# Optimization experiments

Hardware: AMD Instinct MI355X
Metric: run time of the kernel (lower is better)

The kernel has to match this reference:

```python
import jax, jax.numpy as jnp
import numpy as np

GI_DIM = 1220
HID = 150
GIJ = 3 * GI_DIM + 60  # 3720


def setup_inputs() -> dict:
    key = jax.random.key(0)
    ks = jax.random.split(key, 16)
    N, P = 50000, 100000
    inp = {
        "g_i": jax.random.normal(ks[0], (N, GI_DIM), jnp.float32),
        "mention_scores": jax.random.normal(ks[1], (N,), jnp.float32),
        "dist_emb": jax.random.normal(ks[2], (9, 20), jnp.float32) * 0.1,
        "genre_emb": jax.random.normal(ks[3], (8, 20), jnp.float32) * 0.1,
        "speaker_emb": jax.random.normal(ks[4], (3, 20), jnp.float32) * 0.1,
        "W1": jax.random.normal(ks[5], (GIJ, HID), jnp.float32) / np.sqrt(GIJ),
        "b1": jnp.zeros((HID,), jnp.float32),
        "W2": jax.random.normal(ks[6], (HID, HID), jnp.float32) / np.sqrt(HID),
        "b2": jnp.zeros((HID,), jnp.float32),
        "W3": jax.random.normal(ks[7], (HID, 1), jnp.float32) / np.sqrt(HID),
        "b3": jnp.zeros((1,), jnp.float32),
        "mention_ids": jax.random.randint(ks[8], (P,), 0, N, jnp.int64 if jax.config.jax_enable_x64 else jnp.int32),
        "antecedent_ids": jax.random.randint(ks[9], (P,), 0, N, jnp.int32),
        "distance_ids": jax.random.randint(ks[10], (P,), 0, 9, jnp.int32),
        "genre_ids": jax.random.randint(ks[11], (P,), 0, 8, jnp.int32),
        "speaker_ids": jax.random.randint(ks[12], (P,), 0, 3, jnp.int32),
    }
    return inp


def reference(g_i, mention_scores, dist_emb, genre_emb, speaker_emb,
              W1, b1, W2, b2, W3, b3,
              mention_ids, antecedent_ids, distance_ids, genre_ids, speaker_ids):
    # phi: [P, 60] pair features (distance, genre, speaker embeddings)
    phi = jnp.concatenate([dist_emb[distance_ids],
                           genre_emb[genre_ids],
                           speaker_emb[speaker_ids]], axis=1)
    i_g = g_i[mention_ids]      # [P, GI_DIM]
    j_g = g_i[antecedent_ids]   # [P, GI_DIM]
    pairs = jnp.concatenate([i_g, j_g, i_g * j_g, phi], axis=1)  # [P, GIJ]
    h = jax.nn.relu(pairs @ W1 + b1)
    h = jax.nn.relu(h @ W2 + b2)
    pairwise = (h @ W3 + b3)[:, 0]  # [P]
    sij = mention_scores[mention_ids] + mention_scores[antecedent_ids] + pairwise
    return sij
```

## Files before the change

kernel.cpp:

```cpp
#include <hip/hip_runtime.h>

#define GI  1220
#define KP  1280
#define BK  128
#define NCH (KP / BK)
#define NP  192
#define ABW 320

typedef _Float16      f16;
typedef _Float16      f16x8 __attribute__((ext_vector_type(8)));
typedef float         f32x4 __attribute__((ext_vector_type(4)));
typedef unsigned int  u32x4 __attribute__((ext_vector_type(4)));
typedef unsigned int  u32x2 __attribute__((ext_vector_type(2)));

__device__ __forceinline__ unsigned short f2h(float f) {
  return __builtin_bit_cast(unsigned short, (f16)f);
}
__device__ __forceinline__ float h2f(unsigned short u) {
  return (float)__builtin_bit_cast(f16, u);
}
__device__ __forceinline__ unsigned int pkh(float a, float b) {
  return (unsigned int)f2h(a) | ((unsigned int)f2h(b) << 16);
}

__global__ void prep_kernel(const float* __restrict__ W1, const float* __restrict__ W2,
                            const float* __restrict__ b1,
                            const float* __restrict__ de, const float* __restrict__ ge,
                            const float* __restrict__ se,
                            unsigned short* __restrict__ W1ab_t,
                            unsigned short* __restrict__ W1c_t,
                            unsigned short* __restrict__ W2_t,
                            float* __restrict__ projs) {
  int idx = blockIdx.x * 256 + threadIdx.x;
  const int R1 = ABW * KP, R2 = NP * KP, R3 = NP * NP, R4 = 20 * NP;
  if (idx < R1) {
    int n = idx / KP, k = idx % KP;
    float v = 0.f;
    if (k < GI) {
      if (n < 150)                 v = W1[k * 150 + n];
      else if (n >= 160 && n < 310) v = W1[(GI + k) * 150 + (n - 160)];
    }
    W1ab_t[idx] = f2h(v);
    return;
  }
  idx -= R1;
  if (idx < R2) {
    int n = idx / KP, k = idx % KP;
    float v = (k < GI && n < 150) ? W1[(2 * GI + k) * 150 + n] : 0.f;
    W1c_t[idx] = f2h(v);
    return;
  }
  idx -= R2;
  if (idx < R3) {
    int n = idx / NP, k = idx % NP;
    float v = (n < 150 && k < 150) ? W2[k * 150 + n] : 0.f;
    W2_t[idx] = f2h(v);
    return;
  }
  idx -= R3;
  if (idx < R4) {
    int r = idx / NP, n = idx % NP;
    float v = 0.f;
    if (n < 150) {
      if (r < 9) {
        v = b1[n];
        for (int t = 0; t < 20; ++t) v += de[r * 20 + t] * W1[(3660 + t) * 150 + n];
      } else if (r < 17) {
        int q = r - 9;
        for (int t = 0; t < 20; ++t) v += ge[q * 20 + t] * W1[(3680 + t) * 150 + n];
      } else {
        int q = r - 17;
        for (int t = 0; t < 20; ++t) v += se[q * 20 + t] * W1[(3700 + t) * 150 + n];
      }
    }
    projs[idx] = v;
  }
}

__global__ __launch_bounds__(256, 3)
void ab_kernel(const float* __restrict__ g, const unsigned short* __restrict__ W1ab_t,
               unsigned short* __restrict__ AB, unsigned short* __restrict__ gb, int N) {
  __shared__ __attribute__((aligned(16))) unsigned short sX[64 * 136];
  const int t = threadIdx.x;
  const int m0 = blockIdx.x * 64;
  const int w = t >> 6, lane = t & 63, quad = lane >> 4, lm = lane & 15;

  f32x4 acc[4][5];
#pragma unroll
  for (int a = 0; a < 4; ++a)
#pragma unroll
    for (int b = 0; b < 5; ++b) { acc[a][b].x = 0.f; acc[a][b].y = 0.f; acc[a][b].z = 0.f; acc[a][b].w = 0.f; }

  const int r = t >> 2, s = t & 3;
  int row = m0 + r; if (row >= N) row = N - 1;
  const float* gr = g + (long)row * GI;
  unsigned short* gbr = gb + (long)row * KP;

  for (int c = 0; c < NCH; ++c) {
    __syncthreads();
#pragma unroll
    for (int i = 0; i < 8; ++i) {
      int k = c * BK + i * 16 + s * 4;
      u32x2 ph; ph.x = 0u; ph.y = 0u;
      if (k < GI) {
        f32x4 x = *(const f32x4*)(gr + k);
        ph.x = pkh(x.x, x.y);
        ph.y = pkh(x.z, x.w);
      }
      *(u32x2*)&sX[r * 136 + i * 16 + s * 4] = ph;
      *(u32x2*)(gbr + k) = ph;
    }
    __syncthreads();
#pragma unroll
    for (int kk = 0; kk < 4; ++kk) {
      f16x8 af[4];
#pragma unroll
      for (int mi = 0; mi < 4; ++mi)
        af[mi] = __builtin_bit_cast(f16x8, *(const u32x4*)&sX[(mi * 16 + lm) * 136 + kk * 32 + quad * 8]);
#pragma unroll
      for (int tl = 0; tl < 5; ++tl) {
        int n = (w * 5 + tl) * 16 + lm;
        f16x8 bfr = __builtin_bit_cast(f16x8, *(const u32x4*)(W1ab_t + n * KP + c * BK + kk * 32 + quad * 8));
#pragma unroll
        for (int mi = 0; mi < 4; ++mi)
          acc[mi][tl] = __builtin_amdgcn_mfma_f32_16x16x32_f16(af[mi], bfr, acc[mi][tl], 0, 0, 0);
      }
    }
  }
#pragma unroll
  for (int mi = 0; mi < 4; ++mi)
#pragma unroll
    for (int reg = 0; reg < 4; ++reg) {
      int m = m0 + mi * 16 + quad * 4 + reg;
      if (m < N) {
#pragma unroll
        for (int tl = 0; tl < 5; ++tl) {
          int n = (w * 5 + tl) * 16 + lm;
          AB[(long)m * ABW + n] = f2h(acc[mi][tl][reg]);
        }
      }
    }
}

__global__ __launch_bounds__(256, 3)
void pair_kernel(const unsigned short* __restrict__ gb, const float* __restrict__ msc,
                 const unsigned short* __restrict__ AB,
                 const unsigned short* __restrict__ W1c_t,
                 const unsigned short* __restrict__ W2_t,
                 const float* __restrict__ projs,
                 const float* __restrict__ b2, const float* __restrict__ W3,
                 const float* __restrict__ b3,
                 const int* __restrict__ mid, const int* __restrict__ aid,
                 const int* __restrict__ did, const int* __restrict__ gid,
                 const int* __restrict__ sid,
                 float* __restrict__ out, int N, int P) {
  __shared__ __attribute__((aligned(16))) unsigned short sXh1[64 * 200];
  __shared__ __attribute__((aligned(16))) unsigned short sBias[64 * NP];
  __shared__ int sM[64], sA[64], sD[64], sG[64], sS[64];
  __shared__ float sScore[64];

  const int t = threadIdx.x;
  const int p0 = blockIdx.x * 64;
  const int w = t >> 6, lane = t & 63, quad = lane >> 4, lm = lane & 15;

  if (t < 64) {
    int p = p0 + t;
    int m_ = 0, a_ = 0, d_ = 0, g_ = 0, s_ = 0;
    float sc = 0.f;
    if (p < P) {
      m_ = mid[p]; a_ = aid[p]; d_ = did[p]; g_ = gid[p]; s_ = sid[p];
      sc = msc[m_] + msc[a_];
    }
    sM[t] = m_; sA[t] = a_; sD[t] = d_; sG[t] = g_; sS[t] = s_;
    sScore[t] = sc;
  }
  __syncthreads();

  const int r = t >> 2, s = t & 3;
  const unsigned short* gbm = gb + (long)sM[r] * KP;
  const unsigned short* gba = gb + (long)sA[r] * KP;

  {
    const unsigned short* Ar = AB + (long)sM[r] * ABW;
    const unsigned short* Br = AB + (long)sA[r] * ABW + 160;
    const float* dp = projs + sD[r] * NP;
    const float* gp = projs + (9 + sG[r]) * NP;
    const float* sp = projs + (17 + sS[r]) * NP;
#pragma unroll
    for (int j = 0; j < 6; ++j) {
      int n = s * 48 + j * 8;
      f32x4 p0v = *(const f32x4*)(dp + n) + *(const f32x4*)(gp + n) + *(const f32x4*)(sp + n);
      f32x4 p1v = *(const f32x4*)(dp + n + 4) + *(const f32x4*)(gp + n + 4) + *(const f32x4*)(sp + n + 4);
      if (n < 160) {
        u32x4 a8 = *(const u32x4*)(Ar + n);
        u32x4 b8 = *(const u32x4*)(Br + n);
        p0v.x += h2f((unsigned short)(a8.x & 0xffff)) + h2f((unsigned short)(b8.x & 0xffff));
        p0v.y += h2f((unsigned short)(a8.x >> 16))    + h2f((unsigned short)(b8.x >> 16));
        p0v.z += h2f((unsigned short)(a8.y & 0xffff)) + h2f((unsigned short)(b8.y & 0xffff));
        p0v.w += h2f((unsigned short)(a8.y >> 16))    + h2f((unsigned short)(b8.y >> 16));
        p1v.x += h2f((unsigned short)(a8.z & 0xffff)) + h2f((unsigned short)(b8.z & 0xffff));
        p1v.y += h2f((unsigned short)(a8.z >> 16))    + h2f((unsigned short)(b8.z >> 16));
        p1v.z += h2f((unsigned short)(a8.w & 0xffff)) + h2f((unsigned short)(b8.w & 0xffff));
        p1v.w += h2f((unsigned short)(a8.w >> 16))    + h2f((unsigned short)(b8.w >> 16));
      }
      u32x4 o;
      o.x = pkh(p0v.x, p0v.y); o.y = pkh(p0v.z, p0v.w);
      o.z = pkh(p1v.x, p1v.y); o.w = pkh(p1v.z, p1v.w);
      *(u32x4*)&sBias[r * NP + n] = o;
    }
  }

  f32x4 acc[4][3];
#pragma unroll
  for (int a = 0; a < 4; ++a)
#pragma unroll
    for (int b = 0; b < 3; ++b) { acc[a][b].x = 0.f; acc[a][b].y = 0.f; acc[a][b].z = 0.f; acc[a][b].w = 0.f; }

  for (int c = 0; c < NCH; ++c) {
    __syncthreads();
#pragma unroll
    for (int i = 0; i < 4; ++i) {
      int k = c * BK + i * 32 + s * 8;
      f16x8 xm = __builtin_bit_cast(f16x8, *(const u32x4*)(gbm + k));
      f16x8 xa = __builtin_bit_cast(f16x8, *(const u32x4*)(gba + k));
      f16x8 pm = xm * xa;
      *(u32x4*)&sXh1[r * 136 + i * 32 + s * 8] = __builtin_bit_cast(u32x4, pm);
    }
    __syncthreads();
#pragma unroll
    for (int kk = 0; kk < 4; ++kk) {
      f16x8 af[4];
#pragma unroll
      for (int mi = 0; mi < 4; ++mi)
        af[mi] = __builtin_bit_cast(f16x8, *(const u32x4*)&sXh1[(mi * 16 + lm) * 136 + kk * 32 + quad * 8]);
#pragma unroll
      for (int tl = 0; tl < 3; ++tl) {
        int n = (w * 3 + tl) * 16 + lm;
        f16x8 bfr = __builtin_bit_cast(f16x8, *(const u32x4*)(W1c_t + n * KP + c * BK + kk * 32 + quad * 8));
#pragma unroll
        for (int mi = 0; mi < 4; ++mi)
          acc[mi][tl] = __builtin_amdgcn_mfma_f32_16x16x32_f16(af[mi], bfr, acc[mi][tl], 0, 0, 0);
      }
    }
  }

  __syncthreads();
#pragma unroll
  for (int mi = 0; mi < 4; ++mi)
#pragma unroll
    for (int tl = 0; tl < 3; ++tl) {
      int n = (w * 3 + tl) * 16 + lm;
#pragma unroll
      for (int reg = 0; reg < 4; ++reg) {
        int m = mi * 16 + quad * 4 + reg;
        float v = acc[mi][tl][reg] + h2f(sBias[m * NP + n]);
        v = fmaxf(v, 0.f);
        sXh1[m * 200 + n] = f2h(v);
      }
    }
  __syncthreads();

  f32x4 acc2[4][3];
#pragma unroll
  for (int a = 0; a < 4; ++a)
#pragma unroll
    for (int b = 0; b < 3; ++b) { acc2[a][b].x = 0.f; acc2[a][b].y = 0.f; acc2[a][b].z = 0.f; acc2[a][b].w = 0.f; }
#pragma unroll
  for (int kk = 0; kk < 6; ++kk) {
    f16x8 af[4];
#pragma unroll
    for (int mi = 0; mi < 4; ++mi)
      af[mi] = __builtin_bit_cast(f16x8, *(const u32x4*)&sXh1[(mi * 16 + lm) * 200 + kk * 32 + quad * 8]);
#pragma unroll
    for (int tl = 0; tl < 3; ++tl) {
      int n = (w * 3 + tl) * 16 + lm;
      f16x8 bfr = __builtin_bit_cast(f16x8, *(const u32x4*)(W2_t + n * NP + kk * 32 + quad * 8));
#pragma unroll
      for (int mi = 0; mi < 4; ++mi)
        acc2[mi][tl] = __builtin_amdgcn_mfma_f32_16x16x32_f16(af[mi], bfr, acc2[mi][tl], 0, 0, 0);
    }
  }

#pragma unroll
  for (int mi = 0; mi < 4; ++mi)
#pragma unroll
    for (int tl = 0; tl < 3; ++tl) {
      int n = (w * 3 + tl) * 16 + lm;
      float bb = (n < 150) ? b2[n] : 0.f;
#pragma unroll
      for (int reg = 0; reg < 4; ++reg) {
        int m = mi * 16 + quad * 4 + reg;
        float v = acc2[mi][tl][reg] + bb;
        v = fmaxf(v, 0.f);
        sBias[m * NP + n] = f2h(v);
      }
    }
  __syncthreads();

  {
    float sum = 0.f;
#pragma unroll
    for (int j = 0; j < 48; ++j) {
      int n = s * 48 + j;
      if (n < 150) sum += h2f(sBias[r * NP + n]) * W3[n];
    }
    sum += __shfl_xor(sum, 1);
    sum += __shfl_xor(sum, 2);
    if (s == 0) {
      int p = p0 + r;
      if (p < P) out[p] = sScore[r] + sum + b3[0];
    }
  }
}

extern "C" void kernel_launch(void* const* d_in, const int* in_sizes, int n_in,
                              void* d_out, int out_size, void* d_ws, size_t ws_size,
                              hipStream_t stream) {
  (void)n_in; (void)out_size; (void)ws_size;
  const float* g   = (const float*)d_in[0];
  const float* msc = (const float*)d_in[1];
  const float* de  = (const float*)d_in[2];
  const float* ge  = (const float*)d_in[3];
  const float* se  = (const float*)d_in[4];
  const float* W1  = (const float*)d_in[5];
  const float* b1  = (const float*)d_in[6];
  const float* W2  = (const float*)d_in[7];
  const float* b2  = (const float*)d_in[8];
  const float* W3  = (const float*)d_in[9];
  const float* b3  = (const float*)d_in[10];
  const int* mid = (const int*)d_in[11];
  const int* aid = (const int*)d_in[12];
  const int* did = (const int*)d_in[13];
  const int* gid = (const int*)d_in[14];
  const int* sid = (const int*)d_in[15];
  const int N = in_sizes[0] / GI;
  const int P = in_sizes[11];
  float* out = (float*)d_out;

  char* ws = (char*)d_ws;
  size_t off = 0;
  auto alloc = [&](size_t bytes) { char* p = ws + off; off = (off + bytes + 255) & ~(size_t)255; return p; };
  unsigned short* gb     = (unsigned short*)alloc((size_t)N * KP * 2);
  unsigned short* AB     = (unsigned short*)alloc((size_t)N * ABW * 2);
  unsigned short* W1ab_t = (unsigned short*)alloc((size_t)ABW * KP * 2);
  unsigned short* W1c_t  = (unsigned short*)alloc((size_t)NP * KP * 2);
  unsigned short* W2_t   = (unsigned short*)alloc((size_t)NP * NP * 2);
  float* projs           = (float*)alloc((size_t)20 * NP * 4);

  const int prep_total = ABW * KP + NP * KP + NP * NP + 20 * NP;
  prep_kernel<<<(prep_total + 255) / 256, 256, 0, stream>>>(W1, W2, b1, de, ge, se,
                                                            W1ab_t, W1c_t, W2_t, projs);
  ab_kernel<<<(N + 63) / 64, 256, 0, stream>>>(g, W1ab_t, AB, gb, N);
  pair_kernel<<<(P + 63) / 64, 256, 0, stream>>>(gb, msc, AB, W1c_t, W2_t, projs,
                                                 b2, W3, b3, mid, aid, did, gid, sid,
                                                 out, N, P);
}
```

Measured before the change: 781.5 us.

## Split fp16 conversion kernel, double-buffer ab_kernel, register-direct pair GEMM with prefetch

Moves the fp32-to-fp16 conversion of g into its own g2h kernel, so ab_kernel now reads fp16 rows and double-buffers them in shared memory with a single barrier per chunk. In pair_kernel, the elementwise product of gathered rows no longer goes through shared memory. Each wave loads its own 16 pair rows straight into registers as MFMA A fragments, with the next chunk prefetched, and computes all 12 N-tiles. This removes two barriers per K-chunk and the LDS round-trip. The cost is an extra kernel launch, an extra pass over g, more registers for 12 accumulators, and less reuse of W1c loads across rows.

Measured after the change: 1.032 ms. +32.1%, slower.

```diff
diff --git a/kernel.cpp b/kernel.cpp
--- a/kernel.cpp
+++ b/kernel.cpp
@@ -21,6 +21,29 @@
 }
 __device__ __forceinline__ unsigned int pkh(float a, float b) {
   return (unsigned int)f2h(a) | ((unsigned int)f2h(b) << 16);
+}
+
+__global__ void g2h_kernel(const float* __restrict__ g, unsigned short* __restrict__ gb,
+                           int N) {
+  int idx = blockIdx.x * 256 + threadIdx.x;
+  if (idx >= N * (KP / 8)) return;
+  int row = idx / (KP / 8);
+  int k = (idx % (KP / 8)) * 8;
+  const float* gr = g + (long)row * GI + k;
+  u32x4 o;
+  if (k + 8 <= GI) {
+    f32x4 a = *(const f32x4*)gr;
+    f32x4 b = *(const f32x4*)(gr + 4);
+    o.x = pkh(a.x, a.y); o.y = pkh(a.z, a.w);
+    o.z = pkh(b.x, b.y); o.w = pkh(b.z, b.w);
+  } else if (k < GI) {
+    f32x4 a = *(const f32x4*)gr;
+    o.x = pkh(a.x, a.y); o.y = pkh(a.z, a.w);
+    o.z = 0u; o.w = 0u;
+  } else {
+    o.x = 0u; o.y = 0u; o.z = 0u; o.w = 0u;
+  }
+  *(u32x4*)(gb + (long)row * KP + k) = o;
 }
 
 __global__ void prep_kernel(const float* __restrict__ W1, const float* __restrict__ W2,
@@ -78,9 +101,10 @@
 }
 
 __global__ __launch_bounds__(256, 3)
-void ab_kernel(const float* __restrict__ g, const unsigned short* __restrict__ W1ab_t,
-               unsigned short* __restrict__ AB, unsigned short* __restrict__ gb, int N) {
-  __shared__ __attribute__((aligned(16))) unsigned short sX[64 * 136];
+void ab_kernel(const unsigned short* __restrict__ gb,
+               const unsigned short* __restrict__ W1ab_t,
+               unsigned short* __restrict__ AB, int N) {
+  __shared__ __attribute__((aligned(16))) unsigned short sX[2][64 * 136];
   const int t = threadIdx.x;
   const int m0 = blockIdx.x * 64;
   const int w = t >> 6, lane = t & 63, quad = lane >> 4, lm = lane & 15;
@@ -93,39 +117,37 @@
 
   const int r = t >> 2, s = t & 3;
   int row = m0 + r; if (row >= N) row = N - 1;
-  const float* gr = g + (long)row * GI;
-  unsigned short* gbr = gb + (long)row * KP;
+  const unsigned short* gr = gb + (long)row * KP;
+
+#pragma unroll
+  for (int q = 0; q < 4; ++q)
+    *(u32x4*)&sX[0][r * 136 + s * 32 + q * 8] = *(const u32x4*)(gr + s * 32 + q * 8);
+  __syncthreads();
 
   for (int c = 0; c < NCH; ++c) {
-    __syncthreads();
-#pragma unroll
-    for (int i = 0; i < 8; ++i) {
-      int k = c * BK + i * 16 + s * 4;
-      u32x2 ph; ph.x = 0u; ph.y = 0u;
-      if (k < GI) {
-        f32x4 x = *(const f32x4*)(gr + k);
-        ph.x = pkh(x.x, x.y);
-        ph.y = pkh(x.z, x.w);
-      }
-      *(u32x2*)&sX[r * 136 + i * 16 + s * 4] = ph;
-      *(u32x2*)(gbr + k) = ph;
-    }
-    __syncthreads();
+    const int cur = c & 1;
+    if (c + 1 < NCH) {
+#pragma unroll
+      for (int q = 0; q < 4; ++q)
+        *(u32x4*)&sX[cur ^ 1][r * 136 + s * 32 + q * 8] =
+            *(const u32x4*)(gr + (c + 1) * BK + s * 32 + q * 8);
+    }
 #pragma unroll
     for (int kk = 0; kk < 4; ++kk) {
       f16x8 af[4];
 #pragma unroll
       for (int mi = 0; mi < 4; ++mi)
-        af[mi] = __builtin_bit_cast(f16x8, *(const u32x4*)&sX[(mi * 16 + lm) * 136 + kk * 32 + quad * 8]);
+        af[mi] = *(const f16x8*)&sX[cur][(mi * 16 + lm) * 136 + kk * 32 + quad * 8];
 #pragma unroll
       for (int tl = 0; tl < 5; ++tl) {
         int n = (w * 5 + tl) * 16 + lm;
-        f16x8 bfr = __builtin_bit_cast(f16x8, *(const u32x4*)(W1ab_t + n * KP + c * BK + kk * 32 + quad * 8));
+        f16x8 bfr = *(const f16x8*)(W1ab_t + n * KP + c * BK + kk * 32 + quad * 8);
 #pragma unroll
         for (int mi = 0; mi < 4; ++mi)
           acc[mi][tl] = __builtin_amdgcn_mfma_f32_16x16x32_f16(af[mi], bfr, acc[mi][tl], 0, 0, 0);
       }
     }
+    __syncthreads();
   }
 #pragma unroll
   for (int mi = 0; mi < 4; ++mi)
@@ -140,6 +162,27 @@
         }
       }
     }
+}
+
+__device__ __forceinline__ void pref(const unsigned short* pm, const unsigned short* pa,
+                                     int ko, f16x8 (&xm)[4], f16x8 (&xa)[4]) {
+#pragma unroll
+  for (int kk = 0; kk < 4; ++kk) {
+    xm[kk] = *(const f16x8*)(pm + ko + kk * 32);
+    xa[kk] = *(const f16x8*)(pa + ko + kk * 32);
+  }
+}
+__device__ __forceinline__ void comp(const unsigned short* __restrict__ W1c_t, int lm, int ko,
+                                     f16x8 (&xm)[4], f16x8 (&xa)[4], f32x4 (&acc)[12]) {
+#pragma unroll
+  for (int kk = 0; kk < 4; ++kk) {
+    f16x8 af = xm[kk] * xa[kk];
+#pragma unroll
+    for (int tl = 0; tl < 12; ++tl) {
+      f16x8 bf = *(const f16x8*)(W1c_t + (tl * 16 + lm) * KP + ko + kk * 32);
+      acc[tl] = __builtin_amdgcn_mfma_f32_16x16x32_f16(af, bf, acc[tl], 0, 0, 0);
+    }
+  }
 }
 
 __global__ __launch_bounds__(256, 3)
@@ -154,7 +197,7 @@
                  const int* __restrict__ did, const int* __restrict__ gid,
                  const int* __restrict__ sid,
                  float* __restrict__ out, int N, int P) {
-  __shared__ __attribute__((aligned(16))) unsigned short sXh1[64 * 200];
+  __shared__ __attribute__((aligned(16))) unsigned short sH1[64 * 200];
   __shared__ __attribute__((aligned(16))) unsigned short sBias[64 * NP];
   __shared__ int sM[64], sA[64], sD[64], sG[64], sS[64];
   __shared__ float sScore[64];
@@ -177,8 +220,6 @@
   __syncthreads();
 
   const int r = t >> 2, s = t & 3;
-  const unsigned short* gbm = gb + (long)sM[r] * KP;
-  const unsigned short* gba = gb + (long)sA[r] * KP;
 
   {
     const unsigned short* Ar = AB + (long)sM[r] * ABW;
@@ -210,71 +251,54 @@
     }
   }
 
-  f32x4 acc[4][3];
+  const int prow = w * 16 + lm;
+  const unsigned short* pm = gb + (long)sM[prow] * KP;
+  const unsigned short* pa = gb + (long)sA[prow] * KP;
+
+  f32x4 acc[12];
+#pragma unroll
+  for (int tl = 0; tl < 12; ++tl) { acc[tl].x = 0.f; acc[tl].y = 0.f; acc[tl].z = 0.f; acc[tl].w = 0.f; }
+
+  const int qo = quad * 8;
+  f16x8 xm0[4], xa0[4], xm1[4], xa1[4];
+  pref(pm, pa, qo, xm0, xa0);
+#pragma unroll
+  for (int c = 0; c < NCH; c += 2) {
+    if (c + 1 < NCH) pref(pm, pa, (c + 1) * BK + qo, xm1, xa1);
+    comp(W1c_t, lm, c * BK + qo, xm0, xa0, acc);
+    if (c + 2 < NCH) pref(pm, pa, (c + 2) * BK + qo, xm0, xa0);
+    if (c + 1 < NCH) comp(W1c_t, lm, (c + 1) * BK + qo, xm1, xa1, acc);
+  }
+
+  __syncthreads();
+#pragma unroll
+  for (int tl = 0; tl < 12; ++tl) {
+    int n = tl * 16 + lm;
+#pragma unroll
+    for (int reg = 0; reg < 4; ++reg) {
+      int m = w * 16 + quad * 4 + reg;
+      float v = acc[tl][reg] + h2f(sBias[m * NP + n]);
+      v = fmaxf(v, 0.f);
+      sH1[m * 200 + n] = f2h(v);
+    }
+  }
+  __syncthreads();
+
+  f32x4 acc2[4][3];
 #pragma unroll
   for (int a = 0; a < 4; ++a)
 #pragma unroll
-    for (int b = 0; b < 3; ++b) { acc[a][b].x = 0.f; acc[a][b].y = 0.f; acc[a][b].z = 0.f; acc[a][b].w = 0.f; }
-
-  for (int c = 0; c < NCH; ++c) {
-    __syncthreads();
-#pragma unroll
-    for (int i = 0; i < 4; ++i) {
-      int k = c * BK + i * 32 + s * 8;
-      f16x8 xm = __builtin_bit_cast(f16x8, *(const u32x4*)(gbm + k));
-      f16x8 xa = __builtin_bit_cast(f16x8, *(const u32x4*)(gba + k));
-      f16x8 pm = xm * xa;
-      *(u32x4*)&sXh1[r * 136 + i * 32 + s * 8] = __builtin_bit_cast(u32x4, pm);
-    }
-    __syncthreads();
-#pragma unroll
-    for (int kk = 0; kk < 4; ++kk) {
-      f16x8 af[4];
-#pragma unroll
-      for (int mi = 0; mi < 4; ++mi)
-        af[mi] = __builtin_bit_cast(f16x8, *(const u32x4*)&sXh1[(mi * 16 + lm) * 136 + kk * 32 + quad * 8]);
-#pragma unroll
-      for (int tl = 0; tl < 3; ++tl) {
-        int n = (w * 3 + tl) * 16 + lm;
-        f16x8 bfr = __builtin_bit_cast(f16x8, *(const u32x4*)(W1c_t + n * KP + c * BK + kk * 32 + quad * 8));
-#pragma unroll
-        for (int mi = 0; mi < 4; ++mi)
-          acc[mi][tl] = __builtin_amdgcn_mfma_f32_16x16x32_f16(af[mi], bfr, acc[mi][tl], 0, 0, 0);
-      }
-    }
-  }
-
-  __syncthreads();
-#pragma unroll
-  for (int mi = 0; mi < 4; ++mi)
+    for (int b = 0; b < 3; ++b) { acc2[a][b].x = 0.f; acc2[a][b].y = 0.f; acc2[a][b].z = 0.f; acc2[a][b].w = 0.f; }
+#pragma unroll
+  for (int kk = 0; kk < 6; ++kk) {
+    f16x8 af[4];
+#pragma unroll
+    for (int mi = 0; mi < 4; ++mi)
+      af[mi] = *(const f16x8*)&sH1[(mi * 16 + lm) * 200 + kk * 32 + qo];
 #pragma unroll
     for (int tl = 0; tl < 3; ++tl) {
       int n = (w * 3 + tl) * 16 + lm;
-#pragma unroll
-      for (int reg = 0; reg < 4; ++reg) {
-        int m = mi * 16 + quad * 4 + reg;
-        float v = acc[mi][tl][reg] + h2f(sBias[m * NP + n]);
-        v = fmaxf(v, 0.f);
-        sXh1[m * 200 + n] = f2h(v);
-      }
-    }
-  __syncthreads();
-
-  f32x4 acc2[4][3];
-#pragma unroll
-  for (int a = 0; a < 4; ++a)
-#pragma unroll
-    for (int b = 0; b < 3; ++b) { acc2[a][b].x = 0.f; acc2[a][b].y = 0.f; acc2[a][b].z = 0.f; acc2[a][b].w = 0.f; }
-#pragma unroll
-  for (int kk = 0; kk < 6; ++kk) {
-    f16x8 af[4];
-#pragma unroll
-    for (int mi = 0; mi < 4; ++mi)
-      af[mi] = __builtin_bit_cast(f16x8, *(const u32x4*)&sXh1[(mi * 16 + lm) * 200 + kk * 32 + quad * 8]);
-#pragma unroll
-    for (int tl = 0; tl < 3; ++tl) {
-      int n = (w * 3 + tl) * 16 + lm;
-      f16x8 bfr = __builtin_bit_cast(f16x8, *(const u32x4*)(W2_t + n * NP + kk * 32 + quad * 8));
+      f16x8 bfr = *(const f16x8*)(W2_t + n * NP + kk * 32 + qo);
 #pragma unroll
       for (int mi = 0; mi < 4; ++mi)
         acc2[mi][tl] = __builtin_amdgcn_mfma_f32_16x16x32_f16(af[mi], bfr, acc2[mi][tl], 0, 0, 0);
@@ -350,7 +374,8 @@
   const int prep_total = ABW * KP + NP * KP + NP * NP + 20 * NP;
   prep_kernel<<<(prep_total + 255) / 256, 256, 0, stream>>>(W1, W2, b1, de, ge, se,
                                                             W1ab_t, W1c_t, W2_t, projs);
-  ab_kernel<<<(N + 63) / 64, 256, 0, stream>>>(g, W1ab_t, AB, gb, N);
+  g2h_kernel<<<(N * (KP / 8) + 255) / 256, 256, 0, stream>>>(g, gb, N);
+  ab_kernel<<<(N + 63) / 64, 256, 0, stream>>>(gb, W1ab_t, AB, N);
   pair_kernel<<<(P + 63) / 64, 256, 0, stream>>>(gb, msc, AB, W1c_t, W2_t, projs,
                                                  b2, W3, b3, mid, aid, did, gid, sid,
                                                  out, N, P);
```

## Split fp16 conversion into own kernel and double-buffer ab/pair GEMM loads

Applied to the files above, without the earlier changes.

Moves the fp32-to-fp16 conversion of g_i out of ab_kernel into a separate g2h_kernel. ab_kernel then reads the fp16 copy with a register-prefetched, double-buffered LDS pipeline. pair_kernel's gathered-row loop now prefetches the next chunk's mention and antecedent rows into registers while the current chunk's MFMAs run, aiming to hide global gather latency. This costs an extra kernel launch, a second read of the fp16 g buffer, and more registers, which may lower occupancy under launch_bounds(256,3).

New measurement: 730.8 us. 1.07x faster.

```diff
diff --git a/kernel.cpp b/kernel.cpp
--- a/kernel.cpp
+++ b/kernel.cpp
@@ -21,6 +21,29 @@
 }
 __device__ __forceinline__ unsigned int pkh(float a, float b) {
   return (unsigned int)f2h(a) | ((unsigned int)f2h(b) << 16);
+}
+
+__global__ void g2h_kernel(const float* __restrict__ g, unsigned short* __restrict__ gb,
+                           int N) {
+  int idx = blockIdx.x * 256 + threadIdx.x;
+  if (idx >= N * (KP / 8)) return;
+  int row = idx / (KP / 8);
+  int k = (idx % (KP / 8)) * 8;
+  const float* gr = g + (long)row * GI + k;
+  u32x4 o;
+  if (k + 8 <= GI) {
+    f32x4 a = *(const f32x4*)gr;
+    f32x4 b = *(const f32x4*)(gr + 4);
+    o.x = pkh(a.x, a.y); o.y = pkh(a.z, a.w);
+    o.z = pkh(b.x, b.y); o.w = pkh(b.z, b.w);
+  } else if (k < GI) {
+    f32x4 a = *(const f32x4*)gr;
+    o.x = pkh(a.x, a.y); o.y = pkh(a.z, a.w);
+    o.z = 0u; o.w = 0u;
+  } else {
+    o.x = 0u; o.y = 0u; o.z = 0u; o.w = 0u;
+  }
+  *(u32x4*)(gb + (long)row * KP + k) = o;
 }
 
 __global__ void prep_kernel(const float* __restrict__ W1, const float* __restrict__ W2,
@@ -78,9 +101,10 @@
 }
 
 __global__ __launch_bounds__(256, 3)
-void ab_kernel(const float* __restrict__ g, const unsigned short* __restrict__ W1ab_t,
-               unsigned short* __restrict__ AB, unsigned short* __restrict__ gb, int N) {
-  __shared__ __attribute__((aligned(16))) unsigned short sX[64 * 136];
+void ab_kernel(const unsigned short* __restrict__ gb,
+               const unsigned short* __restrict__ W1ab_t,
+               unsigned short* __restrict__ AB, int N) {
+  __shared__ __attribute__((aligned(16))) unsigned short sX[2][64 * 136];
   const int t = threadIdx.x;
   const int m0 = blockIdx.x * 64;
   const int w = t >> 6, lane = t & 63, quad = lane >> 4, lm = lane & 15;
@@ -93,40 +117,46 @@
 
   const int r = t >> 2, s = t & 3;
   int row = m0 + r; if (row >= N) row = N - 1;
-  const float* gr = g + (long)row * GI;
-  unsigned short* gbr = gb + (long)row * KP;
+  const unsigned short* gr = gb + (long)row * KP;
+
+  u32x4 xr[4];
+  auto loadx = [&](int c) {
+#pragma unroll
+    for (int q = 0; q < 4; ++q)
+      xr[q] = *(const u32x4*)(gr + c * BK + s * 32 + q * 8);
+  };
+  auto storex = [&](int buf) {
+#pragma unroll
+    for (int q = 0; q < 4; ++q)
+      *(u32x4*)&sX[buf][r * 136 + s * 32 + q * 8] = xr[q];
+  };
+
+  loadx(0);
+  storex(0);
+  __syncthreads();
 
   for (int c = 0; c < NCH; ++c) {
-    __syncthreads();
-#pragma unroll
-    for (int i = 0; i < 8; ++i) {
-      int k = c * BK + i * 16 + s * 4;
-      u32x2 ph; ph.x = 0u; ph.y = 0u;
-      if (k < GI) {
-        f32x4 x = *(const f32x4*)(gr + k);
-        ph.x = pkh(x.x, x.y);
-        ph.y = pkh(x.z, x.w);
-      }
-      *(u32x2*)&sX[r * 136 + i * 16 + s * 4] = ph;
-      *(u32x2*)(gbr + k) = ph;
-    }
-    __syncthreads();
+    const int cur = c & 1;
+    if (c + 1 < NCH) loadx(c + 1);
 #pragma unroll
     for (int kk = 0; kk < 4; ++kk) {
       f16x8 af[4];
 #pragma unroll
       for (int mi = 0; mi < 4; ++mi)
-        af[mi] = __builtin_bit_cast(f16x8, *(const u32x4*)&sX[(mi * 16 + lm) * 136 + kk * 32 + quad * 8]);
+        af[mi] = *(const f16x8*)&sX[cur][(mi * 16 + lm) * 136 + kk * 32 + quad * 8];
 #pragma unroll
       for (int tl = 0; tl < 5; ++tl) {
         int n = (w * 5 + tl) * 16 + lm;
-        f16x8 bfr = __builtin_bit_cast(f16x8, *(const u32x4*)(W1ab_t + n * KP + c * BK + kk * 32 + quad * 8));
+        f16x8 bfr = *(const f16x8*)(W1ab_t + n * KP + c * BK + kk * 32 + quad * 8);
 #pragma unroll
         for (int mi = 0; mi < 4; ++mi)
           acc[mi][tl] = __builtin_amdgcn_mfma_f32_16x16x32_f16(af[mi], bfr, acc[mi][tl], 0, 0, 0);
       }
     }
-  }
+    if (c + 1 < NCH) storex(cur ^ 1);
+    __syncthreads();
+  }
+
 #pragma unroll
   for (int mi = 0; mi < 4; ++mi)
 #pragma unroll
@@ -216,32 +246,52 @@
 #pragma unroll
     for (int b = 0; b < 3; ++b) { acc[a][b].x = 0.f; acc[a][b].y = 0.f; acc[a][b].z = 0.f; acc[a][b].w = 0.f; }
 
-  for (int c = 0; c < NCH; ++c) {
-    __syncthreads();
+  u32x4 xm0[4], xa0[4], xm1[4], xa1[4];
+  auto loadc = [&](int c, u32x4 (&xm)[4], u32x4 (&xa)[4]) {
 #pragma unroll
     for (int i = 0; i < 4; ++i) {
-      int k = c * BK + i * 32 + s * 8;
-      f16x8 xm = __builtin_bit_cast(f16x8, *(const u32x4*)(gbm + k));
-      f16x8 xa = __builtin_bit_cast(f16x8, *(const u32x4*)(gba + k));
-      f16x8 pm = xm * xa;
+      xm[i] = *(const u32x4*)(gbm + c * BK + i * 32 + s * 8);
+      xa[i] = *(const u32x4*)(gba + c * BK + i * 32 + s * 8);
+    }
+  };
+  auto storec = [&](u32x4 (&xm)[4], u32x4 (&xa)[4]) {
+#pragma unroll
+    for (int i = 0; i < 4; ++i) {
+      f16x8 pm = __builtin_bit_cast(f16x8, xm[i]) * __builtin_bit_cast(f16x8, xa[i]);
       *(u32x4*)&sXh1[r * 136 + i * 32 + s * 8] = __builtin_bit_cast(u32x4, pm);
     }
-    __syncthreads();
+  };
+  auto mfmac = [&](int c) {
 #pragma unroll
     for (int kk = 0; kk < 4; ++kk) {
       f16x8 af[4];
 #pragma unroll
       for (int mi = 0; mi < 4; ++mi)
-        af[mi] = __builtin_bit_cast(f16x8, *(const u32x4*)&sXh1[(mi * 16 + lm) * 136 + kk * 32 + quad * 8]);
+        af[mi] = *(const f16x8*)&sXh1[(mi * 16 + lm) * 136 + kk * 32 + quad * 8];
 #pragma unroll
       for (int tl = 0; tl < 3; ++tl) {
         int n = (w * 3 + tl) * 16 + lm;
-        f16x8 bfr = __builtin_bit_cast(f16x8, *(const u32x4*)(W1c_t + n * KP + c * BK + kk * 32 + quad * 8));
+        f16x8 bfr = *(const f16x8*)(W1c_t + n * KP + c * BK + kk * 32 + quad * 8);
 #pragma unroll
         for (int mi = 0; mi < 4; ++mi)
           acc[mi][tl] = __builtin_amdgcn_mfma_f32_16x16x32_f16(af[mi], bfr, acc[mi][tl], 0, 0, 0);
       }
     }
+  };
+
+  loadc(0, xm0, xa0);
+#pragma unroll
+  for (int c = 0; c < NCH; c += 2) {
+    if (c + 1 < NCH) loadc(c + 1, xm1, xa1);
+    __syncthreads();
+    storec(xm0, xa0);
+    __syncthreads();
+    mfmac(c);
+    if (c + 2 < NCH) loadc(c + 2, xm0, xa0);
+    __syncthreads();
+    storec(xm1, xa1);
+    __syncthreads();
+    mfmac(c + 1);
   }
 
   __syncthreads();
@@ -270,11 +320,11 @@
     f16x8 af[4];
 #pragma unroll
     for (int mi = 0; mi < 4; ++mi)
-      af[mi] = __builtin_bit_cast(f16x8, *(const u32x4*)&sXh1[(mi * 16 + lm) * 200 + kk * 32 + quad * 8]);
+      af[mi] = *(const f16x8*)&sXh1[(mi * 16 + lm) * 200 + kk * 32 + quad * 8];
 #pragma unroll
     for (int tl = 0; tl < 3; ++tl) {
       int n = (w * 3 + tl) * 16 + lm;
-      f16x8 bfr = __builtin_bit_cast(f16x8, *(const u32x4*)(W2_t + n * NP + kk * 32 + quad * 8));
+      f16x8 bfr = *(const f16x8*)(W2_t + n * NP + kk * 32 + quad * 8);
 #pragma unroll
       for (int mi = 0; mi < 4; ++mi)
         acc2[mi][tl] = __builtin_amdgcn_mfma_f32_16x16x32_f16(af[mi], bfr, acc2[mi][tl], 0, 0, 0);
@@ -350,7 +400,8 @@
   const int prep_total = ABW * KP + NP * KP + NP * NP + 20 * NP;
   prep_kernel<<<(prep_total + 255) / 256, 256, 0, stream>>>(W1, W2, b1, de, ge, se,
                                                             W1ab_t, W1c_t, W2_t, projs);
-  ab_kernel<<<(N + 63) / 64, 256, 0, stream>>>(g, W1ab_t, AB, gb, N);
+  g2h_kernel<<<(N * (KP / 8) + 255) / 256, 256, 0, stream>>>(g, gb, N);
+  ab_kernel<<<(N + 63) / 64, 256, 0, stream>>>(gb, W1ab_t, AB, N);
   pair_kernel<<<(P + 63) / 64, 256, 0, stream>>>(gb, msc, AB, W1c_t, W2_t, projs,
                                                  b2, W3, b3, mid, aid, did, gid, sid,
                                                  out, N, P);
```
